# Kernel tuning notes

Hardware: AMD Instinct MI355X
Metric: run time of the kernel (lower is better)

Reference implementation:

```python
import jax, jax.numpy as jnp
import numpy as np

B, T, C, H = 2, 2048, 1024, 16
D = C // H  # head dim = 64


def setup_inputs() -> dict:
    key = jax.random.key(0)
    k1, k2, k3 = jax.random.split(key, 3)
    s = 1.0 / np.sqrt(C)
    return {
        "x": jax.random.normal(k1, (B, T, C), dtype=jnp.float32),
        "w_qkv": jax.random.normal(k2, (C, 3 * C), dtype=jnp.float32) * s,
        "b_qkv": jnp.zeros((3 * C,), dtype=jnp.float32),
        "w_proj": jax.random.normal(k3, (C, C), dtype=jnp.float32) * s,
        "b_proj": jnp.zeros((C,), dtype=jnp.float32),
    }


def reference(x, w_qkv, b_qkv, w_proj, b_proj):
    Bx, Tx, Cx = x.shape
    qkv = x @ w_qkv + b_qkv                      # [B,T,3C]
    q, k, v = jnp.split(qkv, 3, axis=-1)         # each [B,T,C]
    # split heads -> [B,H,T,D]
    q = q.reshape(Bx, Tx, H, D).transpose(0, 2, 1, 3)
    k = k.reshape(Bx, Tx, H, D).transpose(0, 2, 1, 3)
    v = v.reshape(Bx, Tx, H, D).transpose(0, 2, 1, 3)
    att = jnp.einsum("bhqd,bhkd->bhqk", q, k) * (1.0 / np.sqrt(D))
    causal = jnp.tril(jnp.ones((Tx, Tx), dtype=bool))
    att = jnp.where(causal, att, -jnp.inf)
    att = jax.nn.softmax(att, axis=-1)
    y = jnp.einsum("bhqk,bhkd->bhqd", att, v)    # [B,H,T,D]
    y = y.transpose(0, 2, 1, 3).reshape(Bx, Tx, Cx)
    return y @ w_proj + b_proj
```

## Files before the change

### kernel.cpp

```cpp
#include <hip/hip_runtime.h>


typedef __attribute__((ext_vector_type(8))) __bf16 bf16x8;
typedef __attribute__((ext_vector_type(4))) float f32x4;
typedef __attribute__((ext_vector_type(8))) unsigned short u16x8;
typedef __attribute__((ext_vector_type(4))) unsigned short u16x4;

#define GAS __attribute__((address_space(1)))
#define LAS __attribute__((address_space(3)))

__device__ __forceinline__ unsigned short f2b(float f) {
  unsigned int u = __float_as_uint(f);
  unsigned int r = 0x7FFFu + ((u >> 16) & 1u);
  return (unsigned short)((u + r) >> 16);
}


__global__ void cvt_f32_to_bf16(const float* __restrict__ src,
                                unsigned short* __restrict__ dst, int n4) {
  int i = blockIdx.x * blockDim.x + threadIdx.x;
  if (i < n4) {
    float4 v = ((const float4*)src)[i];
    u16x4 o = { f2b(v.x), f2b(v.y), f2b(v.z), f2b(v.w) };
    *(u16x4*)(dst + (size_t)i * 4) = o;
  }
}

__global__ void transpose_f32_to_bf16(const float* __restrict__ src,
                                      unsigned short* __restrict__ dst,
                                      int K, int N) {
  __shared__ float tile[32][33];
  int n0 = blockIdx.x * 32, k0 = blockIdx.y * 32;
  int tx = threadIdx.x, ty = threadIdx.y;
#pragma unroll
  for (int i = 0; i < 32; i += 8)
    tile[ty + i][tx] = src[(size_t)(k0 + ty + i) * N + n0 + tx];
  __syncthreads();
#pragma unroll
  for (int i = 0; i < 32; i += 8)
    dst[(size_t)(n0 + ty + i) * K + k0 + tx] = f2b(tile[tx][ty + i]);
}


template <int MODE>
__global__ void __launch_bounds__(256) gemm_bt(
    const unsigned short* __restrict__ A, const unsigned short* __restrict__ Bt,
    const float* __restrict__ bias,
    unsigned short* __restrict__ Oq, unsigned short* __restrict__ Ok,
    unsigned short* __restrict__ Ov, float* __restrict__ Of,
    int M, int N, int K) {
  __shared__ unsigned short As[2 * 128 * 64];
  __shared__ unsigned short Bs[2 * 128 * 64];

  const int tid = threadIdx.x;
  const int lane = tid & 63;
  const int wid = tid >> 6;
  const int wr = wid >> 1, wc = wid & 1;
  const int lr = lane & 15, lg = lane >> 4;
  const int m0 = blockIdx.x * 128;
  const int n0 = blockIdx.y * 128;

  f32x4 acc[4][4];
#pragma unroll
  for (int mi = 0; mi < 4; mi++)
#pragma unroll
    for (int ni = 0; ni < 4; ni++) acc[mi][ni] = (f32x4){0.f, 0.f, 0.f, 0.f};

  auto stage = [&](int t, int buf) {
    const int k0 = t * 64;
    unsigned short* Ad = As + buf * (128 * 64);
    unsigned short* Bd = Bs + buf * (128 * 64);
#pragma unroll
    for (int it = 0; it < 4; ++it) {
      const int chunk_u = it * 256 + (tid & ~63);
      const int chunk = chunk_u + lane;
      const int row = chunk >> 3;
      const int col = ((chunk & 7) ^ (row & 7)) * 8;
      __builtin_amdgcn_global_load_lds(
          (GAS unsigned int*)(A + (size_t)(m0 + row) * K + k0 + col),
          (LAS unsigned int*)(Ad + chunk_u * 8), 16, 0, 0);
      __builtin_amdgcn_global_load_lds(
          (GAS unsigned int*)(Bt + (size_t)(n0 + row) * K + k0 + col),
          (LAS unsigned int*)(Bd + chunk_u * 8), 16, 0, 0);
    }
  };

  const int swa = (lr & 7) * 8;
  const int kt = K >> 6;

  stage(0, 0);

  for (int t = 0; t < kt; ++t) {
    const int cur = t & 1;
    __builtin_amdgcn_s_barrier();
    if (t + 1 < kt) {
      stage(t + 1, cur ^ 1);
      asm volatile("s_waitcnt vmcnt(8)" ::: "memory");
    } else {
      asm volatile("s_waitcnt vmcnt(0)" ::: "memory");
    }
    __builtin_amdgcn_s_barrier();

    const unsigned short* Ab = As + cur * (128 * 64);
    const unsigned short* Bb = Bs + cur * (128 * 64);

#pragma unroll
    for (int kk = 0; kk < 2; ++kk) {
      bf16x8 af[4], bfr[4];
#pragma unroll
      for (int mi = 0; mi < 4; mi++)
        af[mi] = *(const bf16x8*)(Ab + (wr * 64 + mi * 16 + lr) * 64 +
                                  ((kk * 32 + lg * 8) ^ swa));
#pragma unroll
      for (int ni = 0; ni < 4; ni++)
        bfr[ni] = *(const bf16x8*)(Bb + (wc * 64 + ni * 16 + lr) * 64 +
                                   ((kk * 32 + lg * 8) ^ swa));
#pragma unroll
      for (int mi = 0; mi < 4; mi++)
#pragma unroll
        for (int ni = 0; ni < 4; ni++)
          acc[mi][ni] = __builtin_amdgcn_mfma_f32_16x16x32_bf16(
              af[mi], bfr[ni], acc[mi][ni], 0, 0, 0);
    }
  }

  const float SCLQ = 0.125f * 1.44269504088896340736f;

#pragma unroll
  for (int mi = 0; mi < 4; mi++) {
#pragma unroll
    for (int ni = 0; ni < 4; ni++) {
      const int nn = n0 + wc * 64 + ni * 16 + lr;
      const float bv = bias[nn];
#pragma unroll
      for (int r = 0; r < 4; r++) {
        const int mm = m0 + wr * 64 + mi * 16 + lg * 4 + r;
        float v = acc[mi][ni][r] + bv;
        if constexpr (MODE == 0) {
          const int b = mm >> 11, tt = mm & 2047;
          const int which = nn >> 10, c = nn & 1023;
          const int h = c >> 6, d = c & 63;
          size_t off;
          if (which == 2)
            off = ((size_t)(b * 16 + h) * 64 + d) * 2048 + tt;
          else
            off = ((size_t)(b * 16 + h) * 2048 + tt) * 64 + d;
          if (which == 0) v *= SCLQ;
          unsigned short* dst = (which == 0) ? Oq : ((which == 1) ? Ok : Ov);
          dst[off] = f2b(v);
        } else {
          Of[(size_t)mm * N + nn] = v;
        }
      }
    }
  }
}


__global__ void __launch_bounds__(256) attn_kernel(
    const unsigned short* __restrict__ Qh, const unsigned short* __restrict__ Kh,
    const unsigned short* __restrict__ Vh, unsigned short* __restrict__ yatt) {
  __shared__ unsigned short KsL[2 * 64 * 64];
  __shared__ unsigned short VsL[2 * 64 * 64];
  __shared__ unsigned short Pl[4 * 16 * 72];

  const int tid = threadIdx.x;
  const int lane = tid & 63;
  const int w = tid >> 6;
  const int lr = lane & 15, lg = lane >> 4;

  const int bh = blockIdx.x & 31;
  const int qt = 31 - (blockIdx.x >> 5);
  const int hh = bh & 15;
  const int bb = bh >> 4;
  const int ntiles = qt + 1;

  const size_t head_base = ((size_t)(bb * 16 + hh)) * 2048 * 64;
  const unsigned short* Qg = Qh + head_base;
  const unsigned short* Kg = Kh + head_base;
  const unsigned short* Vg = Vh + head_base;

  const int q0 = qt * 64 + w * 16;

  bf16x8 aq0 = *(const bf16x8*)(Qg + (size_t)(q0 + lr) * 64 + lg * 8);
  bf16x8 aq1 = *(const bf16x8*)(Qg + (size_t)(q0 + lr) * 64 + 32 + lg * 8);

  bf16x8 vones;
#pragma unroll
  for (int j = 0; j < 8; j++) vones[j] = (__bf16)1.0f;

  float m_run[4], l_run[4];
  f32x4 acc_o[4];
#pragma unroll
  for (int r = 0; r < 4; r++) { m_run[r] = -__builtin_inff(); l_run[r] = 0.f; }
#pragma unroll
  for (int dj = 0; dj < 4; dj++) acc_o[dj] = (f32x4){0.f, 0.f, 0.f, 0.f};

  const int sub = lane >> 3;
  const int srccol = (((lane & 7) ^ sub) << 3);

  auto stage = [&](int kv0, int buf) {
    unsigned short* Kd = KsL + buf * (64 * 64);
    unsigned short* Vd = VsL + buf * (64 * 64);
#pragma unroll
    for (int it = 0; it < 2; ++it) {
      const int r0 = it * 32 + w * 8;
      const int row = r0 + sub;
      __builtin_amdgcn_global_load_lds(
          (GAS unsigned int*)(Kg + (size_t)(kv0 + row) * 64 + srccol),
          (LAS unsigned int*)(Kd + r0 * 64), 16, 0, 0);
      __builtin_amdgcn_global_load_lds(
          (GAS unsigned int*)(Vg + (size_t)row * 2048 + kv0 + srccol),
          (LAS unsigned int*)(Vd + r0 * 64), 16, 0, 0);
    }
  };

  __bf16* Pw = (__bf16*)(Pl + w * 16 * 72);
  const int swr = (lr & 7) << 3;

  stage(0, 0);

  for (int i = 0; i < ntiles; ++i) {
    const int cur = i & 1;
    __builtin_amdgcn_s_barrier();
    if (i + 1 < ntiles) {
      stage((i + 1) * 64, cur ^ 1);
      asm volatile("s_waitcnt vmcnt(4)" ::: "memory");
    } else {
      asm volatile("s_waitcnt vmcnt(0)" ::: "memory");
    }
    __builtin_amdgcn_s_barrier();

    const int kv0 = i * 64;
    const unsigned short* Kb = KsL + cur * (64 * 64);
    const unsigned short* Vb = VsL + cur * (64 * 64);

    f32x4 s[4];
#pragma unroll
    for (int nj = 0; nj < 4; nj++) {
      const unsigned short* krow = Kb + (nj * 16 + lr) * 64;
      bf16x8 kb0 = *(const bf16x8*)(krow + ((lg * 8) ^ swr));
      bf16x8 kb1 = *(const bf16x8*)(krow + ((32 + lg * 8) ^ swr));
      f32x4 z = (f32x4){0.f, 0.f, 0.f, 0.f};
      z = __builtin_amdgcn_mfma_f32_16x16x32_bf16(aq0, kb0, z, 0, 0, 0);
      z = __builtin_amdgcn_mfma_f32_16x16x32_bf16(aq1, kb1, z, 0, 0, 0);
      s[nj] = z;
    }

    if (i == ntiles - 1) {
#pragma unroll
      for (int nj = 0; nj < 4; nj++) {
        const int key = kv0 + nj * 16 + lr;
#pragma unroll
        for (int r = 0; r < 4; r++) {
          const int qrow = q0 + lg * 4 + r;
          if (key > qrow) s[nj][r] = -__builtin_inff();
        }
      }
    }

    float pm[4];
#pragma unroll
    for (int r = 0; r < 4; r++)
      pm[r] = fmaxf(fmaxf(s[0][r], s[1][r]), fmaxf(s[2][r], s[3][r]));

    const bool okl = (pm[0] <= m_run[0] + 8.f) & (pm[1] <= m_run[1] + 8.f) &
                     (pm[2] <= m_run[2] + 8.f) & (pm[3] <= m_run[3] + 8.f);
    if (!__all(okl)) {
#pragma unroll
      for (int r = 0; r < 4; r++) {
#pragma unroll
        for (int off = 1; off < 16; off <<= 1)
          pm[r] = fmaxf(pm[r], __shfl_xor(pm[r], off));
        const float mn = fmaxf(m_run[r], pm[r]);
        const float sc = exp2f(m_run[r] - mn);
        m_run[r] = mn;
        l_run[r] *= sc;
#pragma unroll
        for (int dj = 0; dj < 4; dj++) acc_o[dj][r] *= sc;
      }
    }

#pragma unroll
    for (int nj = 0; nj < 4; nj++) {
#pragma unroll
      for (int r = 0; r < 4; r++) {
        const float p = exp2f(s[nj][r] - m_run[r]);
        Pw[(lg * 4 + r) * 72 + nj * 16 + lr] = (__bf16)p;
      }
    }

    bf16x8 pa0 = *(const bf16x8*)(Pw + lr * 72 + lg * 8);
    bf16x8 pa1 = *(const bf16x8*)(Pw + lr * 72 + 32 + lg * 8);

    f32x4 zs = (f32x4){0.f, 0.f, 0.f, 0.f};
    zs = __builtin_amdgcn_mfma_f32_16x16x32_bf16(pa0, vones, zs, 0, 0, 0);
    zs = __builtin_amdgcn_mfma_f32_16x16x32_bf16(pa1, vones, zs, 0, 0, 0);

#pragma unroll
    for (int dj = 0; dj < 4; dj++) {
      const unsigned short* vrow = Vb + (dj * 16 + lr) * 64;
      bf16x8 vb0 = *(const bf16x8*)(vrow + ((lg * 8) ^ swr));
      bf16x8 vb1 = *(const bf16x8*)(vrow + ((32 + lg * 8) ^ swr));
      acc_o[dj] = __builtin_amdgcn_mfma_f32_16x16x32_bf16(pa0, vb0, acc_o[dj], 0, 0, 0);
      acc_o[dj] = __builtin_amdgcn_mfma_f32_16x16x32_bf16(pa1, vb1, acc_o[dj], 0, 0, 0);
    }

#pragma unroll
    for (int r = 0; r < 4; r++) l_run[r] += zs[r];
  }

  __bf16* yb = (__bf16*)yatt;
#pragma unroll
  for (int r = 0; r < 4; r++) {
    const float inv = 1.0f / l_run[r];
    const int t = q0 + lg * 4 + r;
    const size_t rowbase = ((size_t)(bb * 2048 + t)) * 1024 + hh * 64;
#pragma unroll
    for (int dj = 0; dj < 4; dj++)
      yb[rowbase + dj * 16 + lr] = (__bf16)(acc_o[dj][r] * inv);
  }
}


extern "C" void kernel_launch(void* const* d_in, const int* in_sizes, int n_in,
                              void* d_out, int out_size, void* d_ws,
                              size_t ws_size, hipStream_t stream) {
  (void)in_sizes; (void)n_in; (void)out_size; (void)ws_size;
  const float* x      = (const float*)d_in[0];
  const float* w_qkv  = (const float*)d_in[1];
  const float* b_qkv  = (const float*)d_in[2];
  const float* w_proj = (const float*)d_in[3];
  const float* b_proj = (const float*)d_in[4];
  float* out = (float*)d_out;

  unsigned short* ws     = (unsigned short*)d_ws;
  unsigned short* xb     = ws;
  unsigned short* wqkvT  = xb     + (size_t)4096 * 1024;
  unsigned short* wprojT = wqkvT  + (size_t)3072 * 1024;
  unsigned short* Qh     = wprojT + (size_t)1024 * 1024;
  unsigned short* Kh     = Qh     + (size_t)2 * 16 * 2048 * 64;
  unsigned short* Vh     = Kh     + (size_t)2 * 16 * 2048 * 64;
  unsigned short* yatt   = Vh     + (size_t)2 * 16 * 2048 * 64;

  cvt_f32_to_bf16<<<4096, 256, 0, stream>>>(x, xb, 1048576);
  transpose_f32_to_bf16<<<dim3(96, 32), dim3(32, 8), 0, stream>>>(w_qkv, wqkvT, 1024, 3072);
  transpose_f32_to_bf16<<<dim3(32, 32), dim3(32, 8), 0, stream>>>(w_proj, wprojT, 1024, 1024);

  gemm_bt<0><<<dim3(32, 24), 256, 0, stream>>>(xb, wqkvT, b_qkv, Qh, Kh, Vh,
                                               nullptr, 4096, 3072, 1024);
  attn_kernel<<<1024, 256, 0, stream>>>(Qh, Kh, Vh, yatt);
  gemm_bt<1><<<dim3(32, 8), 256, 0, stream>>>(yatt, wprojT, b_proj, nullptr,
                                              nullptr, nullptr, out, 4096, 1024, 1024);
}
```

Before: 127.4 us.

## Stage QKV epilogue through LDS and use 128-row query tiles in attention

The QKV GEMM epilogue now writes its bf16 results into shared memory first, then stores them to the Q/K/V head layouts as coalesced 16-byte vectors. Before, each thread scattered single 2-byte stores, which were strided for the transposed V. The attention kernel now uses 512 threads with 8 waves covering 128 query rows, so each K/V tile staged in LDS serves twice as many queries. Waves in the lower half skip the last tile with a per-wave diagonal check. The cost is more LDS and barrier work per block, half as many blocks, and some idle waves on the final tile.

```diff
diff --git a/kernel.cpp b/kernel.cpp
--- a/kernel.cpp
+++ b/kernel.cpp
@@ -49,8 +49,9 @@
     unsigned short* __restrict__ Oq, unsigned short* __restrict__ Ok,
     unsigned short* __restrict__ Ov, float* __restrict__ Of,
     int M, int N, int K) {
-  __shared__ unsigned short As[2 * 128 * 64];
-  __shared__ unsigned short Bs[2 * 128 * 64];
+  __shared__ unsigned short smem[4 * 128 * 64];
+  unsigned short* As = smem;
+  unsigned short* Bs = smem + 2 * 128 * 64;
 
   const int tid = threadIdx.x;
   const int lane = tid & 63;
@@ -126,43 +127,75 @@
 
   const float SCLQ = 0.125f * 1.44269504088896340736f;
 
-#pragma unroll
-  for (int mi = 0; mi < 4; mi++) {
-#pragma unroll
-    for (int ni = 0; ni < 4; ni++) {
-      const int nn = n0 + wc * 64 + ni * 16 + lr;
-      const float bv = bias[nn];
-#pragma unroll
-      for (int r = 0; r < 4; r++) {
-        const int mm = m0 + wr * 64 + mi * 16 + lg * 4 + r;
-        float v = acc[mi][ni][r] + bv;
-        if constexpr (MODE == 0) {
-          const int b = mm >> 11, tt = mm & 2047;
-          const int which = nn >> 10, c = nn & 1023;
-          const int h = c >> 6, d = c & 63;
-          size_t off;
-          if (which == 2)
-            off = ((size_t)(b * 16 + h) * 64 + d) * 2048 + tt;
-          else
-            off = ((size_t)(b * 16 + h) * 2048 + tt) * 64 + d;
-          if (which == 0) v *= SCLQ;
-          unsigned short* dst = (which == 0) ? Oq : ((which == 1) ? Ok : Ov);
-          dst[off] = f2b(v);
-        } else {
-          Of[(size_t)mm * N + nn] = v;
-        }
-      }
-    }
-  }
-}
-
-
-__global__ void __launch_bounds__(256) attn_kernel(
+  if constexpr (MODE == 1) {
+#pragma unroll
+    for (int mi = 0; mi < 4; mi++) {
+#pragma unroll
+      for (int ni = 0; ni < 4; ni++) {
+        const int nn = n0 + wc * 64 + ni * 16 + lr;
+        const float bv = bias[nn];
+#pragma unroll
+        for (int r = 0; r < 4; r++) {
+          const int mm = m0 + wr * 64 + mi * 16 + lg * 4 + r;
+          Of[(size_t)mm * N + nn] = acc[mi][ni][r] + bv;
+        }
+      }
+    }
+  } else {
+    unsigned short* L = smem;
+    const int which = n0 >> 10;
+    const float sc = (which == 0) ? SCLQ : 1.0f;
+    __syncthreads();
+#pragma unroll
+    for (int mi = 0; mi < 4; mi++) {
+#pragma unroll
+      for (int ni = 0; ni < 4; ni++) {
+        const int nn_l = wc * 64 + ni * 16 + lr;
+        const float bv = bias[n0 + nn_l];
+#pragma unroll
+        for (int r = 0; r < 4; r++) {
+          const int mm_l = wr * 64 + mi * 16 + lg * 4 + r;
+          const unsigned short v = f2b((acc[mi][ni][r] + bv) * sc);
+          if (which == 2) L[nn_l * 136 + mm_l] = v;
+          else            L[mm_l * 136 + nn_l] = v;
+        }
+      }
+    }
+    __syncthreads();
+    const int b = m0 >> 11;
+    const int t0 = m0 & 2047;
+    const int h0 = (n0 & 1023) >> 6;
+    if (which == 2) {
+      const int row = tid >> 1;
+      const int hsub = row >> 6, d = row & 63;
+      const int tt0 = (tid & 1) * 64;
+      const unsigned short* src = L + row * 136 + tt0;
+      unsigned short* dst = Ov +
+          ((size_t)((b * 16 + h0 + hsub) * 64 + d)) * 2048 + t0 + tt0;
+#pragma unroll
+      for (int j = 0; j < 8; j++)
+        *(u16x8*)(dst + j * 8) = *(const u16x8*)(src + j * 8);
+    } else {
+      const int mm_l = tid & 127;
+      const int hsub = tid >> 7;
+      const unsigned short* src = L + mm_l * 136 + hsub * 64;
+      unsigned short* base = (which == 0) ? Oq : Ok;
+      unsigned short* dst = base +
+          ((size_t)(b * 16 + h0 + hsub) * 2048 + t0 + mm_l) * 64;
+#pragma unroll
+      for (int j = 0; j < 8; j++)
+        *(u16x8*)(dst + j * 8) = *(const u16x8*)(src + j * 8);
+    }
+  }
+}
+
+
+__global__ void __launch_bounds__(512) attn_kernel(
     const unsigned short* __restrict__ Qh, const unsigned short* __restrict__ Kh,
     const unsigned short* __restrict__ Vh, unsigned short* __restrict__ yatt) {
   __shared__ unsigned short KsL[2 * 64 * 64];
   __shared__ unsigned short VsL[2 * 64 * 64];
-  __shared__ unsigned short Pl[4 * 16 * 72];
+  __shared__ unsigned short Pl[8 * 16 * 72];
 
   const int tid = threadIdx.x;
   const int lane = tid & 63;
@@ -170,17 +203,18 @@
   const int lr = lane & 15, lg = lane >> 4;
 
   const int bh = blockIdx.x & 31;
-  const int qt = 31 - (blockIdx.x >> 5);
+  const int qt = 15 - (blockIdx.x >> 5);
   const int hh = bh & 15;
   const int bb = bh >> 4;
-  const int ntiles = qt + 1;
+  const int ntiles = 2 * qt + 2;
+  const int diagw = 2 * qt + ((w >> 2) & 1);
 
   const size_t head_base = ((size_t)(bb * 16 + hh)) * 2048 * 64;
   const unsigned short* Qg = Qh + head_base;
   const unsigned short* Kg = Kh + head_base;
   const unsigned short* Vg = Vh + head_base;
 
-  const int q0 = qt * 64 + w * 16;
+  const int q0 = qt * 128 + w * 16;
 
   bf16x8 aq0 = *(const bf16x8*)(Qg + (size_t)(q0 + lr) * 64 + lg * 8);
   bf16x8 aq1 = *(const bf16x8*)(Qg + (size_t)(q0 + lr) * 64 + 32 + lg * 8);
@@ -196,23 +230,19 @@
 #pragma unroll
   for (int dj = 0; dj < 4; dj++) acc_o[dj] = (f32x4){0.f, 0.f, 0.f, 0.f};
 
-  const int sub = lane >> 3;
-  const int srccol = (((lane & 7) ^ sub) << 3);
+  const int srow = tid >> 3;
+  const int scol = (((tid & 7) ^ (srow & 7)) << 3);
 
   auto stage = [&](int kv0, int buf) {
     unsigned short* Kd = KsL + buf * (64 * 64);
     unsigned short* Vd = VsL + buf * (64 * 64);
-#pragma unroll
-    for (int it = 0; it < 2; ++it) {
-      const int r0 = it * 32 + w * 8;
-      const int row = r0 + sub;
-      __builtin_amdgcn_global_load_lds(
-          (GAS unsigned int*)(Kg + (size_t)(kv0 + row) * 64 + srccol),
-          (LAS unsigned int*)(Kd + r0 * 64), 16, 0, 0);
-      __builtin_amdgcn_global_load_lds(
-          (GAS unsigned int*)(Vg + (size_t)row * 2048 + kv0 + srccol),
-          (LAS unsigned int*)(Vd + r0 * 64), 16, 0, 0);
-    }
+    const int base_u = (tid & ~63) * 8;
+    __builtin_amdgcn_global_load_lds(
+        (GAS unsigned int*)(Kg + (size_t)(kv0 + srow) * 64 + scol),
+        (LAS unsigned int*)(Kd + base_u), 16, 0, 0);
+    __builtin_amdgcn_global_load_lds(
+        (GAS unsigned int*)(Vg + (size_t)srow * 2048 + kv0 + scol),
+        (LAS unsigned int*)(Vd + base_u), 16, 0, 0);
   };
 
   __bf16* Pw = (__bf16*)(Pl + w * 16 * 72);
@@ -225,89 +255,91 @@
     __builtin_amdgcn_s_barrier();
     if (i + 1 < ntiles) {
       stage((i + 1) * 64, cur ^ 1);
-      asm volatile("s_waitcnt vmcnt(4)" ::: "memory");
+      asm volatile("s_waitcnt vmcnt(2)" ::: "memory");
     } else {
       asm volatile("s_waitcnt vmcnt(0)" ::: "memory");
     }
     __builtin_amdgcn_s_barrier();
 
-    const int kv0 = i * 64;
-    const unsigned short* Kb = KsL + cur * (64 * 64);
-    const unsigned short* Vb = VsL + cur * (64 * 64);
-
-    f32x4 s[4];
-#pragma unroll
-    for (int nj = 0; nj < 4; nj++) {
-      const unsigned short* krow = Kb + (nj * 16 + lr) * 64;
-      bf16x8 kb0 = *(const bf16x8*)(krow + ((lg * 8) ^ swr));
-      bf16x8 kb1 = *(const bf16x8*)(krow + ((32 + lg * 8) ^ swr));
-      f32x4 z = (f32x4){0.f, 0.f, 0.f, 0.f};
-      z = __builtin_amdgcn_mfma_f32_16x16x32_bf16(aq0, kb0, z, 0, 0, 0);
-      z = __builtin_amdgcn_mfma_f32_16x16x32_bf16(aq1, kb1, z, 0, 0, 0);
-      s[nj] = z;
-    }
-
-    if (i == ntiles - 1) {
+    if (i <= diagw) {
+      const int kv0 = i * 64;
+      const unsigned short* Kb = KsL + cur * (64 * 64);
+      const unsigned short* Vb = VsL + cur * (64 * 64);
+
+      f32x4 s[4];
 #pragma unroll
       for (int nj = 0; nj < 4; nj++) {
-        const int key = kv0 + nj * 16 + lr;
+        const unsigned short* krow = Kb + (nj * 16 + lr) * 64;
+        bf16x8 kb0 = *(const bf16x8*)(krow + ((lg * 8) ^ swr));
+        bf16x8 kb1 = *(const bf16x8*)(krow + ((32 + lg * 8) ^ swr));
+        f32x4 z = (f32x4){0.f, 0.f, 0.f, 0.f};
+        z = __builtin_amdgcn_mfma_f32_16x16x32_bf16(aq0, kb0, z, 0, 0, 0);
+        z = __builtin_amdgcn_mfma_f32_16x16x32_bf16(aq1, kb1, z, 0, 0, 0);
+        s[nj] = z;
+      }
+
+      if (i == diagw) {
+#pragma unroll
+        for (int nj = 0; nj < 4; nj++) {
+          const int key = kv0 + nj * 16 + lr;
+#pragma unroll
+          for (int r = 0; r < 4; r++) {
+            const int qrow = q0 + lg * 4 + r;
+            if (key > qrow) s[nj][r] = -__builtin_inff();
+          }
+        }
+      }
+
+      float pm[4];
+#pragma unroll
+      for (int r = 0; r < 4; r++)
+        pm[r] = fmaxf(fmaxf(s[0][r], s[1][r]), fmaxf(s[2][r], s[3][r]));
+
+      const bool okl = (pm[0] <= m_run[0] + 8.f) & (pm[1] <= m_run[1] + 8.f) &
+                       (pm[2] <= m_run[2] + 8.f) & (pm[3] <= m_run[3] + 8.f);
+      if (!__all(okl)) {
 #pragma unroll
         for (int r = 0; r < 4; r++) {
-          const int qrow = q0 + lg * 4 + r;
-          if (key > qrow) s[nj][r] = -__builtin_inff();
-        }
-      }
-    }
-
-    float pm[4];
-#pragma unroll
-    for (int r = 0; r < 4; r++)
-      pm[r] = fmaxf(fmaxf(s[0][r], s[1][r]), fmaxf(s[2][r], s[3][r]));
-
-    const bool okl = (pm[0] <= m_run[0] + 8.f) & (pm[1] <= m_run[1] + 8.f) &
-                     (pm[2] <= m_run[2] + 8.f) & (pm[3] <= m_run[3] + 8.f);
-    if (!__all(okl)) {
-#pragma unroll
-      for (int r = 0; r < 4; r++) {
-#pragma unroll
-        for (int off = 1; off < 16; off <<= 1)
-          pm[r] = fmaxf(pm[r], __shfl_xor(pm[r], off));
-        const float mn = fmaxf(m_run[r], pm[r]);
-        const float sc = exp2f(m_run[r] - mn);
-        m_run[r] = mn;
-        l_run[r] *= sc;
-#pragma unroll
-        for (int dj = 0; dj < 4; dj++) acc_o[dj][r] *= sc;
-      }
-    }
-
-#pragma unroll
-    for (int nj = 0; nj < 4; nj++) {
-#pragma unroll
-      for (int r = 0; r < 4; r++) {
-        const float p = exp2f(s[nj][r] - m_run[r]);
-        Pw[(lg * 4 + r) * 72 + nj * 16 + lr] = (__bf16)p;
-      }
-    }
-
-    bf16x8 pa0 = *(const bf16x8*)(Pw + lr * 72 + lg * 8);
-    bf16x8 pa1 = *(const bf16x8*)(Pw + lr * 72 + 32 + lg * 8);
-
-    f32x4 zs = (f32x4){0.f, 0.f, 0.f, 0.f};
-    zs = __builtin_amdgcn_mfma_f32_16x16x32_bf16(pa0, vones, zs, 0, 0, 0);
-    zs = __builtin_amdgcn_mfma_f32_16x16x32_bf16(pa1, vones, zs, 0, 0, 0);
-
-#pragma unroll
-    for (int dj = 0; dj < 4; dj++) {
-      const unsigned short* vrow = Vb + (dj * 16 + lr) * 64;
-      bf16x8 vb0 = *(const bf16x8*)(vrow + ((lg * 8) ^ swr));
-      bf16x8 vb1 = *(const bf16x8*)(vrow + ((32 + lg * 8) ^ swr));
-      acc_o[dj] = __builtin_amdgcn_mfma_f32_16x16x32_bf16(pa0, vb0, acc_o[dj], 0, 0, 0);
-      acc_o[dj] = __builtin_amdgcn_mfma_f32_16x16x32_bf16(pa1, vb1, acc_o[dj], 0, 0, 0);
-    }
-
-#pragma unroll
-    for (int r = 0; r < 4; r++) l_run[r] += zs[r];
+#pragma unroll
+          for (int off = 1; off < 16; off <<= 1)
+            pm[r] = fmaxf(pm[r], __shfl_xor(pm[r], off));
+          const float mn = fmaxf(m_run[r], pm[r]);
+          const float sc = exp2f(m_run[r] - mn);
+          m_run[r] = mn;
+          l_run[r] *= sc;
+#pragma unroll
+          for (int dj = 0; dj < 4; dj++) acc_o[dj][r] *= sc;
+        }
+      }
+
+#pragma unroll
+      for (int nj = 0; nj < 4; nj++) {
+#pragma unroll
+        for (int r = 0; r < 4; r++) {
+          const float p = exp2f(s[nj][r] - m_run[r]);
+          Pw[(lg * 4 + r) * 72 + nj * 16 + lr] = (__bf16)p;
+        }
+      }
+
+      bf16x8 pa0 = *(const bf16x8*)(Pw + lr * 72 + lg * 8);
+      bf16x8 pa1 = *(const bf16x8*)(Pw + lr * 72 + 32 + lg * 8);
+
+      f32x4 zs = (f32x4){0.f, 0.f, 0.f, 0.f};
+      zs = __builtin_amdgcn_mfma_f32_16x16x32_bf16(pa0, vones, zs, 0, 0, 0);
+      zs = __builtin_amdgcn_mfma_f32_16x16x32_bf16(pa1, vones, zs, 0, 0, 0);
+
+#pragma unroll
+      for (int dj = 0; dj < 4; dj++) {
+        const unsigned short* vrow = Vb + (dj * 16 + lr) * 64;
+        bf16x8 vb0 = *(const bf16x8*)(vrow + ((lg * 8) ^ swr));
+        bf16x8 vb1 = *(const bf16x8*)(vrow + ((32 + lg * 8) ^ swr));
+        acc_o[dj] = __builtin_amdgcn_mfma_f32_16x16x32_bf16(pa0, vb0, acc_o[dj], 0, 0, 0);
+        acc_o[dj] = __builtin_amdgcn_mfma_f32_16x16x32_bf16(pa1, vb1, acc_o[dj], 0, 0, 0);
+      }
+
+#pragma unroll
+      for (int r = 0; r < 4; r++) l_run[r] += zs[r];
+    }
   }
 
   __bf16* yb = (__bf16*)yatt;
@@ -349,7 +381,7 @@
 
   gemm_bt<0><<<dim3(32, 24), 256, 0, stream>>>(xb, wqkvT, b_qkv, Qh, Kh, Vh,
                                                nullptr, 4096, 3072, 1024);
-  attn_kernel<<<1024, 256, 0, stream>>>(Qh, Kh, Vh, yatt);
+  attn_kernel<<<512, 512, 0, stream>>>(Qh, Kh, Vh, yatt);
   gemm_bt<1><<<dim3(32, 8), 256, 0, stream>>>(yatt, wprojT, b_proj, nullptr,
                                               nullptr, nullptr, out, 4096, 1024, 1024);
 }
```

Measured after the change: 124.3 us. 2.4% less time.
